# Optimization experiments

Hardware: AMD Instinct MI355X
Metric: run time of the kernel (lower is better)

Reference implementation:

```python
import jax, jax.numpy as jnp
import numpy as np

IMAGE = 800.0
HIGH_THRESH = 0.7   # torchvision RPN fg_iou_thresh
LOW_THRESH = 0.3    # torchvision RPN bg_iou_thresh
BELOW_LOW = -1      # Matcher.BELOW_LOW_THRESHOLD
BETWEEN = -2        # Matcher.BETWEEN_THRESHOLDS


def _make_boxes(key, shape, max_wh):
    # shape = (..., 4) target; build valid xyxy boxes inside the image
    k1, k2 = jax.random.split(key)
    xy = jax.random.uniform(k1, shape[:-1] + (2,)) * (IMAGE - max_wh)
    wh = jax.random.uniform(k2, shape[:-1] + (2,)) * (max_wh - 4.0) + 4.0
    return jnp.concatenate([xy, xy + wh], axis=-1)


def setup_inputs() -> dict:
    key = jax.random.key(0)
    kA, kG, kS, kC = jax.random.split(key, 4)
    B, A, G = 4, 160000, 64
    anchors = _make_boxes(kA, (B, A, 4), 128.0)
    gt_boxes = _make_boxes(kG, (B, G, 4), 200.0)
    # soft score labels in {0, 0.5, 1} style: mostly 1, some <1 (ignored), some 0
    u = jax.random.uniform(kS, (B, G))
    score_labels = jnp.where(u < 0.15, 0.0, jnp.where(u < 0.3, 0.5, 1.0)).astype(jnp.float32)
    confidence_labels = jax.random.randint(kC, (B, G), 0, 2).astype(jnp.int32)
    return {"anchors": anchors, "gt_boxes": gt_boxes,
            "score_labels": score_labels, "confidence_labels": confidence_labels}


def _box_iou(a, b):
    # a: [G,4] gt, b: [A,4] anchors -> [G,A]
    area_a = (a[:, 2] - a[:, 0]) * (a[:, 3] - a[:, 1])          # [G]
    area_b = (b[:, 2] - b[:, 0]) * (b[:, 3] - b[:, 1])          # [A]
    lt = jnp.maximum(a[:, None, :2], b[None, :, :2])            # [G,A,2]
    rb = jnp.minimum(a[:, None, 2:], b[None, :, 2:])            # [G,A,2]
    wh = jnp.clip(rb - lt, 0.0)
    inter = wh[..., 0] * wh[..., 1]                              # [G,A]
    return inter / (area_a[:, None] + area_b[None, :] - inter)


def _matcher(mq):
    # torchvision Matcher with allow_low_quality_matches=True. mq: [G,A]
    matched_vals = mq.max(axis=0)                                # [A]
    matches = mq.argmax(axis=0).astype(jnp.int32)                # [A]
    m = jnp.where(matched_vals < LOW_THRESH, BELOW_LOW,
                  jnp.where(matched_vals < HIGH_THRESH, BETWEEN, matches))
    # restore, for each gt, anchors achieving that gt's max IoU
    highest_per_gt = mq.max(axis=1, keepdims=True)               # [G,1]
    low_quality = (mq == highest_per_gt).any(axis=0)             # [A]
    return jnp.where(low_quality, matches, m)


def _assign_one(anchors, gt, scores, confs):
    mq = _box_iou(gt, anchors)                                   # [G,A]
    midx = _matcher(mq)                                          # [A]
    cl = jnp.clip(midx, 0)
    matched_gt = gt[cl]                                          # [A,4]
    pos = midx >= 0
    labels = pos.astype(jnp.float32)
    labels = jnp.minimum(labels, scores[cl])
    labels = jnp.where(midx == BELOW_LOW, 0.0, labels)
    labels = jnp.where(midx == BETWEEN, -1.0, labels)
    labels = jnp.where((scores[cl] < 1.0) & pos, -1.0, labels)
    labels = jnp.where((confs[cl] == 0) & pos, -1.0, labels)
    return labels, matched_gt


def reference(anchors, gt_boxes, score_labels, confidence_labels):
    labels, matched_gt_boxes = jax.vmap(_assign_one)(anchors, gt_boxes, score_labels, confidence_labels)
    return labels, matched_gt_boxes
```

## Files before the change

### kernel.cpp

```cpp
#include <hip/hip_runtime.h>

constexpr int NB = 4;
constexpr int NA = 160000;
constexpr int NG = 64;

__device__ __forceinline__ float box_area(float x0, float y0, float x1, float y1) {
#pragma clang fp contract(off)
    return (x1 - x0) * (y1 - y0);
}

__device__ __forceinline__ void inter_denom(float gx0, float gy0, float gx1, float gy1, float garea,
                                            float ax0, float ay0, float ax1, float ay1, float aarea,
                                            float& inter, float& denom) {
#pragma clang fp contract(off)
    float ltx = fmaxf(gx0, ax0);
    float lty = fmaxf(gy0, ay0);
    float rbx = fminf(gx1, ax1);
    float rby = fminf(gy1, ay1);
    float w = fmaxf(rbx - ltx, 0.0f);
    float h = fmaxf(rby - lty, 0.0f);
    inter = w * h;
    float s = garea + aarea;
    denom = s - inter;
}

__device__ __forceinline__ float iou_f(float gx0, float gy0, float gx1, float gy1, float garea,
                                       float ax0, float ay0, float ax1, float ay1, float aarea) {
    float inter, denom;
    inter_denom(gx0, gy0, gx1, gy1, garea, ax0, ay0, ax1, ay1, aarea, inter, denom);
    return inter / denom;
}

__device__ __forceinline__ bool frac_gt(float i1, float d1, float i2, float d2) {
    return (double)i1 * (double)d2 > (double)i2 * (double)d1;
}

__global__ __launch_bounds__(256) void k_gt_highest(
        const float* __restrict__ anchors, const float* __restrict__ gts,
        float* __restrict__ highest ) {
    const int b = blockIdx.y;
    const int lane = threadIdx.x & 63;
    const int wid = __builtin_amdgcn_readfirstlane(threadIdx.x >> 6);

    const float4* __restrict__ gt4 = reinterpret_cast<const float4*>(gts) + b * NG;
    const float4* __restrict__ anc = reinterpret_cast<const float4*>(anchors) + (size_t)b * NA;

    float4 g = gt4[lane];
    float garea = box_area(g.x, g.y, g.z, g.w);

    const int base = blockIdx.x * 160 + wid * 40;
    float bi = 0.0f, bd = 1.0f;
#pragma unroll 8
    for (int i = 0; i < 40; ++i) {
        float4 a = anc[base + i];
        float aarea = box_area(a.x, a.y, a.z, a.w);
        float inter, denom;
        inter_denom(g.x, g.y, g.z, g.w, garea, a.x, a.y, a.z, a.w, aarea,
                    inter, denom);
        if (frac_gt(inter, denom, bi, bd)) { bi = inter; bd = denom; }
    }

    __shared__ float pi[4][NG], pd[4][NG];
    pi[wid][lane] = bi;
    pd[wid][lane] = bd;
    __syncthreads();
    if (threadIdx.x < NG) {
        float ci = pi[0][threadIdx.x], cd = pd[0][threadIdx.x];
#pragma unroll
        for (int wv = 1; wv < 4; ++wv) {
            float ni = pi[wv][threadIdx.x], nd = pd[wv][threadIdx.x];
            if (frac_gt(ni, nd, ci, cd)) { ci = ni; cd = nd; }
        }
        float m = ci / cd;
        atomicMax(reinterpret_cast<int*>(&highest[b * NG + threadIdx.x]),
                  __float_as_int(m));
    }
}

__global__ __launch_bounds__(256) void k_assign(
        const float* __restrict__ anchors, const float* __restrict__ gts,
        const float* __restrict__ scores, const int* __restrict__ confs,
        const float* __restrict__ highest,
        float* __restrict__ labels_out, float4* __restrict__ boxes_out) {
    __shared__ float4 sg[NG];
    __shared__ float2 sah[NG];
    __shared__ float ssc[NG];
    __shared__ int scf[NG];

    const int b = blockIdx.y;
    if (threadIdx.x < NG) {
        const int gi = threadIdx.x;
        float4 gv = reinterpret_cast<const float4*>(gts)[b * NG + gi];
        sg[gi] = gv;
        sah[gi] = make_float2(box_area(gv.x, gv.y, gv.z, gv.w),
                              highest[b * NG + gi]);
        ssc[gi] = scores[b * NG + gi];
        scf[gi] = confs[b * NG + gi];
    }
    __syncthreads();

    const int ai = blockIdx.x * 256 + threadIdx.x;
    const float4* __restrict__ anc = reinterpret_cast<const float4*>(anchors) + (size_t)b * NA;
    float4 av = anc[ai];
    float aarea = box_area(av.x, av.y, av.z, av.w);

    float best = -1.0f;
    int   matches = 0;
    bool  lowq = false;
#pragma unroll 4
    for (int g = 0; g < NG; ++g) {
        float4 gb = sg[g];
        float2 ah = sah[g];
        float v = iou_f(gb.x, gb.y, gb.z, gb.w, ah.x,
                        av.x, av.y, av.z, av.w, aarea);
        if (v > best) { best = v; matches = g; }
        lowq |= (v == ah.y);
    }

    int m    = (best < 0.3f) ? -1 : ((best < 0.7f) ? -2 : matches);
    int midx = lowq ? matches : m;
    int cl   = (midx < 0) ? 0 : midx;

    float4 mg = sg[cl];
    float  sc = ssc[cl];
    int    cf = scf[cl];

    bool pos = (midx >= 0);
    float lab = pos ? 1.0f : 0.0f;
    lab = fminf(lab, sc);
    if (midx == -1) lab = 0.0f;
    if (midx == -2) lab = -1.0f;
    if (sc < 1.0f && pos) lab = -1.0f;
    if (cf == 0 && pos) lab = -1.0f;

    labels_out[(size_t)b * NA + ai] = lab;
    boxes_out[(size_t)b * NA + ai] = mg;
}

extern "C" void kernel_launch(void* const* d_in, const int* in_sizes, int n_in,
                              void* d_out, int out_size, void* d_ws, size_t ws_size,
                              hipStream_t stream) {
    const float* anchors = (const float*)d_in[0];
    const float* gts     = (const float*)d_in[1];
    const float* scores  = (const float*)d_in[2];
    const int*   confs   = (const int*)d_in[3];

    float* labels_out = (float*)d_out;
    float4* boxes_out = (float4*)((float*)d_out + (size_t)NB * NA);
    float* highest = (float*)d_ws;

    hipMemsetAsync(d_ws, 0, (size_t)NB * NG * sizeof(float), stream);

    dim3 g1(1000, NB), g2(625, NB), blk(256);
    k_gt_highest<<<g1, blk, 0, stream>>>(anchors, gts, highest);
    k_assign<<<g2, blk, 0, stream>>>(anchors, gts, scores, confs, highest,
                                     labels_out, boxes_out);
}
```

Before: 142.3 us.

## Fuse memset, gt-max and assign into one cooperative kernel with grid syncs

Replaces the memset plus two kernel launches with a single cooperative kernel of 1000 blocks. Each block zeroes or reduces per-gt max IoU, then grid-syncs twice and performs assignment on its own anchor slice. The double-precision fraction compare is replaced by an fp32 two-product compare, and the IEEE division by a reciprocal with Newton refinement. This removes launch gaps and fp64 work, but adds grid-barrier cost and relies on enough blocks being co-resident; the old path is kept as a fallback if the cooperative launch fails.

```diff
diff --git a/kernel.cpp b/kernel.cpp
--- a/kernel.cpp
+++ b/kernel.cpp
@@ -1,8 +1,15 @@
 #include <hip/hip_runtime.h>
+#include <hip/hip_cooperative_groups.h>
+
+namespace cg = cooperative_groups;
 
 constexpr int NB = 4;
 constexpr int NA = 160000;
 constexpr int NG = 64;
+static_assert(NB * NG == 256, "zero phase assumes one thread per ws entry");
+
+constexpr int BPB  = 250;
+constexpr int GRID = NB * BPB;
 
 __device__ __forceinline__ float box_area(float x0, float y0, float x1, float y1) {
 #pragma clang fp contract(off)
@@ -24,15 +31,147 @@
     denom = s - inter;
 }
 
+__device__ __forceinline__ bool frac_gt(float i1, float d1, float i2, float d2) {
+#pragma clang fp contract(off)
+    float p1 = i1 * d2;
+    float p2 = i2 * d1;
+    float e1 = fmaf(i1, d2, -p1);
+    float e2 = fmaf(i2, d1, -p2);
+    return (p1 > p2) || ((p1 == p2) && (e1 > e2));
+}
+
+__device__ __forceinline__ float div_rn(float n, float d) {
+    float y = __builtin_amdgcn_rcpf(d);
+    float e = fmaf(-d, y, 1.0f);
+    y = fmaf(e, y, y);
+    float q = n * y;
+    float r = fmaf(-d, q, n);
+    q = fmaf(r, y, q);
+    float r2 = fmaf(-d, q, n);
+    return fmaf(r2, y, q);
+}
+
+__global__ __launch_bounds__(256, 4) void fused(
+        const float* __restrict__ anchors, const float* __restrict__ gts,
+        const float* __restrict__ scores, const int* __restrict__ confs,
+        int* __restrict__ highest ,
+        float* __restrict__ labels_out, float4* __restrict__ boxes_out) {
+    __shared__ float4 sg[NG];
+    __shared__ float2 sah[NG];
+    __shared__ float  ssc[NG];
+    __shared__ int    scf[NG];
+    __shared__ float  pi[4][NG], pd[4][NG];
+
+    const int bx   = blockIdx.x;
+    const int b    = bx / BPB;
+    const int j    = bx - b * BPB;
+    const int lane = threadIdx.x & 63;
+    const int wid  = __builtin_amdgcn_readfirstlane(threadIdx.x >> 6);
+
+    if (threadIdx.x < NG) {
+        const int gi = threadIdx.x;
+        sg[gi]  = reinterpret_cast<const float4*>(gts)[b * NG + gi];
+        ssc[gi] = scores[b * NG + gi];
+        scf[gi] = confs[b * NG + gi];
+    }
+    if (bx == 0) {
+        __hip_atomic_store(&highest[threadIdx.x], 0, __ATOMIC_RELAXED,
+                           __HIP_MEMORY_SCOPE_AGENT);
+    }
+    cg::grid_group grid = cg::this_grid();
+    grid.sync();
+
+    const float4* __restrict__ anc =
+        reinterpret_cast<const float4*>(anchors) + (size_t)b * NA;
+    float4 g = reinterpret_cast<const float4*>(gts)[b * NG + lane];
+    float garea = box_area(g.x, g.y, g.z, g.w);
+
+    float bi = 0.0f, bd = 1.0f;
+#pragma unroll
+    for (int cc = 0; cc < 4; ++cc) {
+        const int base = (j + cc * BPB) * 160 + wid * 40;
+#pragma unroll 8
+        for (int i = 0; i < 40; ++i) {
+            float4 a = anc[base + i];
+            float aarea = box_area(a.x, a.y, a.z, a.w);
+            float inter, denom;
+            inter_denom(g.x, g.y, g.z, g.w, garea, a.x, a.y, a.z, a.w, aarea,
+                        inter, denom);
+            if (frac_gt(inter, denom, bi, bd)) { bi = inter; bd = denom; }
+        }
+    }
+    pi[wid][lane] = bi;
+    pd[wid][lane] = bd;
+    __syncthreads();
+    if (threadIdx.x < NG) {
+        float ci = pi[0][threadIdx.x], cd = pd[0][threadIdx.x];
+#pragma unroll
+        for (int wv = 1; wv < 4; ++wv) {
+            float ni = pi[wv][threadIdx.x], nd = pd[wv][threadIdx.x];
+            if (frac_gt(ni, nd, ci, cd)) { ci = ni; cd = nd; }
+        }
+        float m = div_rn(ci, cd);
+        atomicMax(&highest[b * NG + threadIdx.x], __float_as_int(m));
+    }
+
+    grid.sync();
+
+    if (threadIdx.x < NG) {
+        const int gi = threadIdx.x;
+        int hv = __hip_atomic_load(&highest[b * NG + gi], __ATOMIC_RELAXED,
+                                   __HIP_MEMORY_SCOPE_AGENT);
+        float4 gv = sg[gi];
+        sah[gi] = make_float2(box_area(gv.x, gv.y, gv.z, gv.w),
+                              __int_as_float(hv));
+    }
+    __syncthreads();
+
+    const int base2 = j * 640;
+    for (int ai = base2 + threadIdx.x; ai < base2 + 640; ai += 256) {
+        float4 av = anc[ai];
+        float aarea = box_area(av.x, av.y, av.z, av.w);
+
+        float best = -1.0f;
+        int   matches = 0;
+        bool  lowq = false;
+#pragma unroll 4
+        for (int gi = 0; gi < NG; ++gi) {
+            float4 gb = sg[gi];
+            float2 ah = sah[gi];
+            float inter, denom;
+            inter_denom(gb.x, gb.y, gb.z, gb.w, ah.x,
+                        av.x, av.y, av.z, av.w, aarea, inter, denom);
+            float v = div_rn(inter, denom);
+            if (v > best) { best = v; matches = gi; }
+            lowq |= (v == ah.y);
+        }
+
+        int m    = (best < 0.3f) ? -1 : ((best < 0.7f) ? -2 : matches);
+        int midx = lowq ? matches : m;
+        int cl   = (midx < 0) ? 0 : midx;
+
+        float4 mg = sg[cl];
+        float  sc = ssc[cl];
+        int    cf = scf[cl];
+
+        bool pos = (midx >= 0);
+        float lab = pos ? 1.0f : 0.0f;
+        lab = fminf(lab, sc);
+        if (midx == -1) lab = 0.0f;
+        if (midx == -2) lab = -1.0f;
+        if (sc < 1.0f && pos) lab = -1.0f;
+        if (cf == 0 && pos) lab = -1.0f;
+
+        labels_out[(size_t)b * NA + ai] = lab;
+        boxes_out[(size_t)b * NA + ai] = mg;
+    }
+}
+
 __device__ __forceinline__ float iou_f(float gx0, float gy0, float gx1, float gy1, float garea,
                                        float ax0, float ay0, float ax1, float ay1, float aarea) {
     float inter, denom;
     inter_denom(gx0, gy0, gx1, gy1, garea, ax0, ay0, ax1, ay1, aarea, inter, denom);
     return inter / denom;
-}
-
-__device__ __forceinline__ bool frac_gt(float i1, float d1, float i2, float d2) {
-    return (double)i1 * (double)d2 > (double)i2 * (double)d1;
 }
 
 __global__ __launch_bounds__(256) void k_gt_highest(
@@ -147,12 +286,20 @@
 
     float* labels_out = (float*)d_out;
     float4* boxes_out = (float4*)((float*)d_out + (size_t)NB * NA);
-    float* highest = (float*)d_ws;
-
-    hipMemsetAsync(d_ws, 0, (size_t)NB * NG * sizeof(float), stream);
-
-    dim3 g1(1000, NB), g2(625, NB), blk(256);
-    k_gt_highest<<<g1, blk, 0, stream>>>(anchors, gts, highest);
-    k_assign<<<g2, blk, 0, stream>>>(anchors, gts, scores, confs, highest,
-                                     labels_out, boxes_out);
-}
+    int* highest_i = (int*)d_ws;
+
+    void* args[] = {(void*)&anchors, (void*)&gts, (void*)&scores, (void*)&confs,
+                    (void*)&highest_i, (void*)&labels_out, (void*)&boxes_out};
+    hipError_t err = hipLaunchCooperativeKernel(
+        fused, dim3(GRID), dim3(256), args, 0u, stream);
+
+    if (err != hipSuccess) {
+        (void)hipGetLastError();
+        float* highest = (float*)d_ws;
+        hipMemsetAsync(d_ws, 0, (size_t)NB * NG * sizeof(float), stream);
+        dim3 g1(1000, NB), g2(625, NB), blk(256);
+        k_gt_highest<<<g1, blk, 0, stream>>>(anchors, gts, highest);
+        k_assign<<<g2, blk, 0, stream>>>(anchors, gts, scores, confs, highest,
+                                         labels_out, boxes_out);
+    }
+}
```

Result: slower. 352.2 us (+147.4%).
